# Performance work log

Hardware: AMD Instinct MI355X
Metric: run time of the kernel (lower is better)

Reference implementation:

```python
import jax, jax.numpy as jnp
import numpy as np

N = 100000   # nodes
E = 1000000  # edges
F = 128      # num_features
H = 64       # hidden_size
C = 1        # num_classes
G = 128      # num graphs in batch


def gcn_conv(x, W, b, src, dst, deg_inv_sqrt):
    # PyG GCNConv: add self-loops, symmetric normalization D^-1/2 (A+I) D^-1/2, then X W + b
    h = x @ W                                   # [N, H]
    norm = deg_inv_sqrt[src] * deg_inv_sqrt[dst]  # [E]
    msg = h[src] * norm[:, None]                # gather + scale, [E, H]
    out = jnp.zeros_like(h).at[dst].add(msg)    # scatter-add to targets
    out = out + h * (deg_inv_sqrt ** 2)[:, None]  # self-loop contribution
    return out + b


def setup_inputs() -> dict:
    key = jax.random.key(0)
    ks = jax.random.split(key, 12)
    x = jax.random.normal(ks[0], (N, F), dtype=jnp.float32)
    edge_index = jax.random.randint(ks[1], (2, E), 0, N, dtype=jnp.int32).astype(jnp.int64)
    batch = jnp.sort(jax.random.randint(ks[2], (N,), 0, G, dtype=jnp.int32)).astype(jnp.int64)
    def glorot(k, fan_in, fan_out):
        s = np.float32(np.sqrt(6.0 / (fan_in + fan_out)))
        return jax.random.uniform(k, (fan_in, fan_out), jnp.float32, -s, s)
    return {
        "x": x, "edge_index": edge_index, "batch": batch,
        "W1": glorot(ks[3], F, H), "b1": jnp.zeros((H,), jnp.float32),
        "W2": glorot(ks[4], H, H), "b2": jnp.zeros((H,), jnp.float32),
        "Wl1": glorot(ks[5], H, H), "bl1": jnp.zeros((H,), jnp.float32),
        "Wl2": glorot(ks[6], H, C), "bl2": jnp.zeros((C,), jnp.float32),
    }


def reference(x, edge_index, batch, W1, b1, W2, b2, Wl1, bl1, Wl2, bl2):
    src, dst = edge_index[0], edge_index[1]
    # degree with self-loops: 1 + in-degree(target)
    deg = jnp.ones((N,), x.dtype).at[dst].add(jnp.ones((E,), x.dtype))
    deg_inv_sqrt = jax.lax.rsqrt(deg)
    h = jax.nn.relu(gcn_conv(x, W1, b1, src, dst, deg_inv_sqrt))
    h = jax.nn.relu(gcn_conv(h, W2, b2, src, dst, deg_inv_sqrt))
    g = jax.ops.segment_sum(h, batch, num_segments=G)  # global_add_pool, [G, H]
    g = jax.nn.relu(g @ Wl1 + bl1)
    out = g @ Wl2 + bl2                                # [G, 1]
    return out.squeeze(axis=1)                         # [G]
```

## Files before the change

### kernel.cpp

```cpp
#include <hip/hip_runtime.h>

#define NN 100000
#define EE 1000000
#define FF 128
#define HH 64
#define GG 128
#define NB 391

__device__ inline unsigned short f2bf(float f) {
    unsigned u = __float_as_uint(f);
    u += 0x7fffu + ((u >> 16) & 1u);
    return (unsigned short)(u >> 16);
}
__device__ inline float bf2f(unsigned short h) {
    return __uint_as_float((unsigned)h << 16);
}

__global__ void k_hist(const int* __restrict__ ei, int* __restrict__ cnt) {
    int e = blockIdx.x * 256 + threadIdx.x;
    if (e < EE) atomicAdd(&cnt[ei[EE + e]], 1);
}

__global__ void k_scan1(const int* __restrict__ cnt, int* __restrict__ part) {
    int i = blockIdx.x * 256 + threadIdx.x;
    int v = (i < NN) ? cnt[i] : 0;
    for (int o = 1; o < 64; o <<= 1) v += __shfl_xor(v, o);
    __shared__ int ws[4];
    if ((threadIdx.x & 63) == 0) ws[threadIdx.x >> 6] = v;
    __syncthreads();
    if (threadIdx.x == 0) part[blockIdx.x] = ws[0] + ws[1] + ws[2] + ws[3];
}

__global__ void k_scan2(int* __restrict__ part) {
    __shared__ int buf[512];
    int t = threadIdx.x;
    int v = (t < NB) ? part[t] : 0;
    buf[t] = v; __syncthreads();
    for (int o = 1; o < 512; o <<= 1) {
        int u = (t >= o) ? buf[t - o] : 0;
        __syncthreads();
        buf[t] += u;
        __syncthreads();
    }
    if (t < NB) part[t] = buf[t] - v;
}

__global__ void k_scan3(const int* __restrict__ cnt, const int* __restrict__ part,
                        int* __restrict__ row_ptr, int* __restrict__ cursor,
                        float* __restrict__ dis) {
    int i = blockIdx.x * 256 + threadIdx.x;
    int v = (i < NN) ? cnt[i] : 0;
    int lane = threadIdx.x & 63, w = threadIdx.x >> 6;
    int incl = v;
    for (int o = 1; o < 64; o <<= 1) { int u = __shfl_up(incl, o); if (lane >= o) incl += u; }
    __shared__ int ws[4];
    if (lane == 63) ws[w] = incl;
    __syncthreads();
    int woff = 0;
    for (int k = 0; k < w; ++k) woff += ws[k];
    int excl = incl - v + woff + part[blockIdx.x];
    if (i < NN) {
        row_ptr[i] = excl;
        cursor[i]  = excl;
        dis[i] = rsqrtf((float)(v + 1));
    }
    if (i == 0) row_ptr[NN] = EE;
}

__global__ void k_place(const int* __restrict__ ei, int* __restrict__ cursor,
                        int* __restrict__ srcs) {
    int e = blockIdx.x * 256 + threadIdx.x;
    if (e < EE) {
        int d = ei[EE + e];
        int p = atomicAdd(&cursor[d], 1);
        srcs[p] = ei[e];
    }
}

template<int K>
__global__ __launch_bounds__(256) void
k_matmul_b(const float* __restrict__ X, const float* __restrict__ W,
           const float* __restrict__ dis, unsigned short* __restrict__ Y) {
    __shared__ float Wl[K * HH];
    for (int i = threadIdx.x; i < K * HH; i += 256) Wl[i] = W[i];
    __syncthreads();
    const int lane = threadIdx.x & 63;
    const int wv   = threadIdx.x >> 6;
    const int c4   = (lane & 15) * 4;
    const int rsg  = lane >> 4;
    const int r0   = blockIdx.x * 64 + wv * 16 + rsg * 4;

    const float* xr0; const float* xr1; const float* xr2; const float* xr3;
    {
        int a = r0,     b_ = r0 + 1, c = r0 + 2, d = r0 + 3;
        if (a > NN - 1) a = NN - 1;
        if (b_ > NN - 1) b_ = NN - 1;
        if (c > NN - 1) c = NN - 1;
        if (d > NN - 1) d = NN - 1;
        xr0 = X + (size_t)a * K; xr1 = X + (size_t)b_ * K;
        xr2 = X + (size_t)c * K; xr3 = X + (size_t)d * K;
    }
    float4 acc0 = {0,0,0,0}, acc1 = {0,0,0,0}, acc2 = {0,0,0,0}, acc3 = {0,0,0,0};

#pragma unroll 8
    for (int k4 = 0; k4 < K / 4; ++k4) {
        const float4 x0 = *(const float4*)(xr0 + k4 * 4);
        const float4 x1 = *(const float4*)(xr1 + k4 * 4);
        const float4 x2 = *(const float4*)(xr2 + k4 * 4);
        const float4 x3 = *(const float4*)(xr3 + k4 * 4);
        const float4 w0 = *(const float4*)&Wl[(k4 * 4 + 0) * HH + c4];
        const float4 w1 = *(const float4*)&Wl[(k4 * 4 + 1) * HH + c4];
        const float4 w2 = *(const float4*)&Wl[(k4 * 4 + 2) * HH + c4];
        const float4 w3 = *(const float4*)&Wl[(k4 * 4 + 3) * HH + c4];
#define FMA4(A, XS) \
        A.x = fmaf(XS.x, w0.x, A.x); A.y = fmaf(XS.x, w0.y, A.y); \
        A.z = fmaf(XS.x, w0.z, A.z); A.w = fmaf(XS.x, w0.w, A.w); \
        A.x = fmaf(XS.y, w1.x, A.x); A.y = fmaf(XS.y, w1.y, A.y); \
        A.z = fmaf(XS.y, w1.z, A.z); A.w = fmaf(XS.y, w1.w, A.w); \
        A.x = fmaf(XS.z, w2.x, A.x); A.y = fmaf(XS.z, w2.y, A.y); \
        A.z = fmaf(XS.z, w2.z, A.z); A.w = fmaf(XS.z, w2.w, A.w); \
        A.x = fmaf(XS.w, w3.x, A.x); A.y = fmaf(XS.w, w3.y, A.y); \
        A.z = fmaf(XS.w, w3.z, A.z); A.w = fmaf(XS.w, w3.w, A.w);
        FMA4(acc0, x0) FMA4(acc1, x1) FMA4(acc2, x2) FMA4(acc3, x3)
#undef FMA4
    }
#define STORE(I, A) { \
        const int r = r0 + I; \
        if (r < NN) { \
            const float d = dis[r]; \
            ushort4 o; \
            o.x = f2bf(A.x * d); o.y = f2bf(A.y * d); \
            o.z = f2bf(A.z * d); o.w = f2bf(A.w * d); \
            *(ushort4*)(Y + (size_t)r * HH + c4) = o; \
        } }
    STORE(0, acc0) STORE(1, acc1) STORE(2, acc2) STORE(3, acc3)
#undef STORE
}

template<bool POOL>
__global__ __launch_bounds__(256) void
k_gconv(const int* __restrict__ row_ptr, const int* __restrict__ srcs,
        const float* __restrict__ dis, const unsigned short* __restrict__ Hs,
        const float* __restrict__ b, float* __restrict__ Out,
        const int* __restrict__ batch, float* __restrict__ g) {
    const int node = blockIdx.x * 4 + (threadIdx.x >> 6);
    const int lane = threadIdx.x & 63;
    const int p1 = row_ptr[node + 1];
    int p = row_ptr[node];
    float a0 = 0.f, a1 = 0.f, a2 = 0.f, a3 = 0.f;
    int s0, s1, s2, s3;
    if (p + 4 <= p1) { s0 = srcs[p]; s1 = srcs[p+1]; s2 = srcs[p+2]; s3 = srcs[p+3]; }
    while (p + 4 <= p1) {
        const int q = p + 4;
        int t0, t1, t2, t3;
        if (q + 4 <= p1) { t0 = srcs[q]; t1 = srcs[q+1]; t2 = srcs[q+2]; t3 = srcs[q+3]; }
        a0 += bf2f(Hs[(size_t)s0 * HH + lane]);
        a1 += bf2f(Hs[(size_t)s1 * HH + lane]);
        a2 += bf2f(Hs[(size_t)s2 * HH + lane]);
        a3 += bf2f(Hs[(size_t)s3 * HH + lane]);
        s0 = t0; s1 = t1; s2 = t2; s3 = t3;
        p = q;
    }
    for (; p < p1; ++p) a0 += bf2f(Hs[(size_t)srcs[p] * HH + lane]);
    float acc = (a0 + a1) + (a2 + a3);
    const float dd = dis[node];
    float v = (acc + bf2f(Hs[(size_t)node * HH + lane])) * dd + b[lane];
    v = fmaxf(v, 0.0f);
    if (POOL) {
        unsafeAtomicAdd(&g[(size_t)batch[node] * HH + lane], v);
    } else {
        Out[(size_t)node * HH + lane] = v;
    }
}

__global__ void k_head1(const float* __restrict__ g, const float* __restrict__ W,
                        const float* __restrict__ b, float* __restrict__ g2) {
    const int idx = blockIdx.x * 256 + threadIdx.x;
    const int row = idx >> 6;
    const int col = idx & 63;
    const float* gr = g + (size_t)row * HH;
    float acc = b[col];
#pragma unroll
    for (int k = 0; k < HH; ++k) acc = fmaf(gr[k], W[k * HH + col], acc);
    g2[idx] = acc > 0.0f ? acc : 0.0f;
}

__global__ void k_head2(const float* __restrict__ g2, const float* __restrict__ W,
                        const float* __restrict__ b, float* __restrict__ out) {
    const int r = threadIdx.x;
    if (r >= GG) return;
    const float* gr = g2 + (size_t)r * HH;
    float acc = 0.0f;
#pragma unroll
    for (int k = 0; k < HH; ++k) acc = fmaf(gr[k], W[k], acc);
    out[r] = acc + b[0];
}

extern "C" void kernel_launch(void* const* d_in, const int* in_sizes, int n_in,
                              void* d_out, int out_size, void* d_ws, size_t ws_size,
                              hipStream_t stream) {
    const float* x   = (const float*)d_in[0];
    const int*   ei  = (const int*)d_in[1];
    const int*   bat = (const int*)d_in[2];
    const float* W1  = (const float*)d_in[3];
    const float* b1  = (const float*)d_in[4];
    const float* W2  = (const float*)d_in[5];
    const float* b2  = (const float*)d_in[6];
    const float* Wl1 = (const float*)d_in[7];
    const float* bl1 = (const float*)d_in[8];
    const float* Wl2 = (const float*)d_in[9];
    const float* bl2 = (const float*)d_in[10];
    float* out = (float*)d_out;

    char* w = (char*)d_ws;
    float* dis     = (float*)(w);
    int*   cnt     = (int*)  (w + 400128);
    int*   row_ptr = (int*)  (w + 800256);
    int*   cursor  = (int*)  (w + 1200640);
    int*   part    = (int*)  (w + 1600768);
    int*   srcs    = (int*)  (w + 1602816);
    unsigned short* B = (unsigned short*)(w + 5602816);
    float* A       = (float*)(w + 31202816);
    float* g       = (float*)(w + 56802816);
    float* g2      = g + GG * HH;

    hipMemsetAsync(cnt, 0, (size_t)NN * sizeof(int), stream);
    k_hist <<<(EE + 255) / 256, 256, 0, stream>>>(ei, cnt);
    k_scan1<<<NB, 256, 0, stream>>>(cnt, part);
    k_scan2<<<1, 512, 0, stream>>>(part);
    k_scan3<<<NB, 256, 0, stream>>>(cnt, part, row_ptr, cursor, dis);
    k_place<<<(EE + 255) / 256, 256, 0, stream>>>(ei, cursor, srcs);

    k_matmul_b<FF><<<(NN + 63) / 64, 256, 0, stream>>>(x, W1, dis, B);
    k_gconv<false><<<NN / 4, 256, 0, stream>>>(row_ptr, srcs, dis, B, b1, A, nullptr, nullptr);

    k_matmul_b<HH><<<(NN + 63) / 64, 256, 0, stream>>>(A, W2, dis, B);
    hipMemsetAsync(g, 0, (size_t)GG * HH * sizeof(float), stream);
    k_gconv<true><<<NN / 4, 256, 0, stream>>>(row_ptr, srcs, dis, B, b2, nullptr, bat, g);

    k_head1<<<(GG * HH) / 256, 256, 0, stream>>>(g, Wl1, bl1, g2);
    k_head2<<<1, 128, 0, stream>>>(g2, Wl2, bl2, out);
}
```

Before: 336.0 us.

## Gather neighbor rows with quarter-wave vector loads and software pipelining

Reorganizes the aggregation so each 16-lane quarter-wave loads a full bf16 row with 8-byte vector loads, processing 8 neighbor rows per batch with the self-loop folded in as an extra item. Index loads and row loads are pipelined one batch ahead, then partial sums are combined with cross-lane shuffles. This aims to raise memory-level parallelism and load width for the random-gather-bound aggregation, at the cost of shuffle reduction overhead and masked wasted loads for low-degree nodes.

```diff
diff --git a/kernel.cpp b/kernel.cpp
--- a/kernel.cpp
+++ b/kernel.cpp
@@ -145,26 +145,66 @@
         const int* __restrict__ batch, float* __restrict__ g) {
     const int node = blockIdx.x * 4 + (threadIdx.x >> 6);
     const int lane = threadIdx.x & 63;
-    const int p1 = row_ptr[node + 1];
-    int p = row_ptr[node];
-    float a0 = 0.f, a1 = 0.f, a2 = 0.f, a3 = 0.f;
-    int s0, s1, s2, s3;
-    if (p + 4 <= p1) { s0 = srcs[p]; s1 = srcs[p+1]; s2 = srcs[p+2]; s3 = srcs[p+3]; }
-    while (p + 4 <= p1) {
-        const int q = p + 4;
-        int t0, t1, t2, t3;
-        if (q + 4 <= p1) { t0 = srcs[q]; t1 = srcs[q+1]; t2 = srcs[q+2]; t3 = srcs[q+3]; }
-        a0 += bf2f(Hs[(size_t)s0 * HH + lane]);
-        a1 += bf2f(Hs[(size_t)s1 * HH + lane]);
-        a2 += bf2f(Hs[(size_t)s2 * HH + lane]);
-        a3 += bf2f(Hs[(size_t)s3 * HH + lane]);
-        s0 = t0; s1 = t1; s2 = t2; s3 = t3;
-        p = q;
-    }
-    for (; p < p1; ++p) a0 += bf2f(Hs[(size_t)srcs[p] * HH + lane]);
-    float acc = (a0 + a1) + (a2 + a3);
+    const int li   = lane & 15;
+    const int qr   = lane >> 4;
+    const int p0   = row_ptr[node];
+    const int deg  = row_ptr[node + 1] - p0;
+    const int items  = deg + 1;
+    const int nbatch = (items + 7) >> 3;
+
+    float ac0 = 0.f, ac1 = 0.f, ac2 = 0.f, ac3 = 0.f;
+
+#define IDX(bi, dA, dB) { \
+        const int iA = 8 * (bi) + qr, iB = iA + 4; \
+        dA = srcs[p0 + (iA < deg ? iA : 0)]; \
+        dB = srcs[p0 + (iB < deg ? iB : 0)]; }
+#define VAL(bi, sA, sB, vA, vB) { \
+        const int iA = 8 * (bi) + qr, iB = iA + 4; \
+        const int rA = (iA < deg) ? sA : node; \
+        const int rB = (iB < deg) ? sB : node; \
+        vA = *(const uint2*)(Hs + (size_t)rA * HH + li * 4); \
+        vB = *(const uint2*)(Hs + (size_t)rB * HH + li * 4); }
+#define CONSUME(bi, vA, vB) { \
+        const int iA = 8 * (bi) + qr, iB = iA + 4; \
+        const unsigned m0 = (iA <= deg) ? vA.x : 0u; \
+        const unsigned m1 = (iA <= deg) ? vA.y : 0u; \
+        const unsigned m2 = (iB <= deg) ? vB.x : 0u; \
+        const unsigned m3 = (iB <= deg) ? vB.y : 0u; \
+        ac0 += bf2f((unsigned short)m0);  ac1 += bf2f((unsigned short)(m0 >> 16)); \
+        ac2 += bf2f((unsigned short)m1);  ac3 += bf2f((unsigned short)(m1 >> 16)); \
+        ac0 += bf2f((unsigned short)m2);  ac1 += bf2f((unsigned short)(m2 >> 16)); \
+        ac2 += bf2f((unsigned short)m3);  ac3 += bf2f((unsigned short)(m3 >> 16)); }
+
+    int sA0, sA1, sB0, sB1;
+    uint2 vA0, vA1;
+    IDX(0, sA0, sA1);
+    VAL(0, sA0, sA1, vA0, vA1);
+    IDX(1, sB0, sB1);
+    for (int bi = 1; bi < nbatch; ++bi) {
+        uint2 vB0, vB1;
+        VAL(bi, sB0, sB1, vB0, vB1);
+        IDX(bi + 1, sB0, sB1);
+        CONSUME(bi - 1, vA0, vA1);
+        vA0 = vB0; vA1 = vB1;
+    }
+    CONSUME(nbatch - 1, vA0, vA1);
+#undef IDX
+#undef VAL
+#undef CONSUME
+
+    ac0 += __shfl_xor(ac0, 16); ac0 += __shfl_xor(ac0, 32);
+    ac1 += __shfl_xor(ac1, 16); ac1 += __shfl_xor(ac1, 32);
+    ac2 += __shfl_xor(ac2, 16); ac2 += __shfl_xor(ac2, 32);
+    ac3 += __shfl_xor(ac3, 16); ac3 += __shfl_xor(ac3, 32);
+    const float c0 = __shfl(ac0, lane >> 2);
+    const float c1 = __shfl(ac1, lane >> 2);
+    const float c2 = __shfl(ac2, lane >> 2);
+    const float c3 = __shfl(ac3, lane >> 2);
+    const int m = lane & 3;
+    float acc = (m == 0) ? c0 : (m == 1) ? c1 : (m == 2) ? c2 : c3;
+
     const float dd = dis[node];
-    float v = (acc + bf2f(Hs[(size_t)node * HH + lane])) * dd + b[lane];
+    float v = acc * dd + b[lane];
     v = fmaxf(v, 0.0f);
     if (POOL) {
         unsafeAtomicAdd(&g[(size_t)batch[node] * HH + lane], v);
```

Result: faster. 319.6 us (-4.9%).

## Pad CSR rows to multiples of four and gather bf16 rows 16 lanes per node

Applied to the files above, without the earlier changes.

The CSR rows are padded to a multiple of four slots. Each row gets the node itself as the self-loop entry, and the rest is filled with a zero dummy row at index NN. The aggregation kernel now handles 16 nodes per block with 16 lanes per node, each lane loading 4 bf16 values (uint2). It stages up to 32 source indices in shared memory and issues up to 32 independent gathers before consuming any, so there are more loads in flight and no tail loop. The costs are extra padded slots, a larger unrolled register footprint, and pooling that now uses four atomics per lane.

```diff
diff --git a/kernel.cpp b/kernel.cpp
--- a/kernel.cpp
+++ b/kernel.cpp
@@ -12,18 +12,17 @@
     u += 0x7fffu + ((u >> 16) & 1u);
     return (unsigned short)(u >> 16);
 }
-__device__ inline float bf2f(unsigned short h) {
-    return __uint_as_float((unsigned)h << 16);
-}
 
 __global__ void k_hist(const int* __restrict__ ei, int* __restrict__ cnt) {
     int e = blockIdx.x * 256 + threadIdx.x;
     if (e < EE) atomicAdd(&cnt[ei[EE + e]], 1);
 }
 
-__global__ void k_scan1(const int* __restrict__ cnt, int* __restrict__ part) {
+__global__ void k_scan1(const int* __restrict__ cnt, int* __restrict__ part,
+                        unsigned short* __restrict__ B) {
+    if (blockIdx.x == 0 && threadIdx.x < HH) B[(size_t)NN * HH + threadIdx.x] = 0;
     int i = blockIdx.x * 256 + threadIdx.x;
-    int v = (i < NN) ? cnt[i] : 0;
+    int v = (i < NN) ? ((cnt[i] + 4) & ~3) : 0;
     for (int o = 1; o < 64; o <<= 1) v += __shfl_xor(v, o);
     __shared__ int ws[4];
     if ((threadIdx.x & 63) == 0) ws[threadIdx.x >> 6] = v;
@@ -47,9 +46,11 @@
 
 __global__ void k_scan3(const int* __restrict__ cnt, const int* __restrict__ part,
                         int* __restrict__ row_ptr, int* __restrict__ cursor,
-                        float* __restrict__ dis) {
+                        int* __restrict__ srcs, float* __restrict__ dis) {
     int i = blockIdx.x * 256 + threadIdx.x;
-    int v = (i < NN) ? cnt[i] : 0;
+    int c = (i < NN) ? cnt[i] : 0;
+    int slots = (c + 4) & ~3;
+    int v = (i < NN) ? slots : 0;
     int lane = threadIdx.x & 63, w = threadIdx.x >> 6;
     int incl = v;
     for (int o = 1; o < 64; o <<= 1) { int u = __shfl_up(incl, o); if (lane >= o) incl += u; }
@@ -61,10 +62,12 @@
     int excl = incl - v + woff + part[blockIdx.x];
     if (i < NN) {
         row_ptr[i] = excl;
-        cursor[i]  = excl;
-        dis[i] = rsqrtf((float)(v + 1));
-    }
-    if (i == 0) row_ptr[NN] = EE;
+        cursor[i]  = excl + 1;
+        srcs[excl] = i;
+        for (int t = c + 1; t < slots; ++t) srcs[excl + t] = NN;
+        dis[i] = rsqrtf((float)(c + 1));
+        if (i == NN - 1) row_ptr[NN] = excl + slots;
+    }
 }
 
 __global__ void k_place(const int* __restrict__ ei, int* __restrict__ cursor,
@@ -137,39 +140,69 @@
 #undef STORE
 }
 
+#define AW(w) __uint_as_float((w) << 16)
+#define AH(w) __uint_as_float((w) & 0xffff0000u)
 template<bool POOL>
 __global__ __launch_bounds__(256) void
 k_gconv(const int* __restrict__ row_ptr, const int* __restrict__ srcs,
         const float* __restrict__ dis, const unsigned short* __restrict__ Hs,
         const float* __restrict__ b, float* __restrict__ Out,
         const int* __restrict__ batch, float* __restrict__ g) {
-    const int node = blockIdx.x * 4 + (threadIdx.x >> 6);
-    const int lane = threadIdx.x & 63;
-    const int p1 = row_ptr[node + 1];
-    int p = row_ptr[node];
-    float a0 = 0.f, a1 = 0.f, a2 = 0.f, a3 = 0.f;
-    int s0, s1, s2, s3;
-    if (p + 4 <= p1) { s0 = srcs[p]; s1 = srcs[p+1]; s2 = srcs[p+2]; s3 = srcs[p+3]; }
-    while (p + 4 <= p1) {
-        const int q = p + 4;
-        int t0, t1, t2, t3;
-        if (q + 4 <= p1) { t0 = srcs[q]; t1 = srcs[q+1]; t2 = srcs[q+2]; t3 = srcs[q+3]; }
-        a0 += bf2f(Hs[(size_t)s0 * HH + lane]);
-        a1 += bf2f(Hs[(size_t)s1 * HH + lane]);
-        a2 += bf2f(Hs[(size_t)s2 * HH + lane]);
-        a3 += bf2f(Hs[(size_t)s3 * HH + lane]);
-        s0 = t0; s1 = t1; s2 = t2; s3 = t3;
-        p = q;
-    }
-    for (; p < p1; ++p) a0 += bf2f(Hs[(size_t)srcs[p] * HH + lane]);
-    float acc = (a0 + a1) + (a2 + a3);
+    __shared__ int L[16 * 32];
+    const int grp  = threadIdx.x >> 4;
+    const int li   = threadIdx.x & 15;
+    const int node = blockIdx.x * 16 + grp;
+    const int p0   = row_ptr[node];
+    const int pend = row_ptr[node + 1];
+    const int slots = pend - p0;
+    const int nbc  = (slots >> 2) < 8 ? (slots >> 2) : 8;
+    int* Lg = L + grp * 32;
+    for (int q = li; q < 32; q += 16)
+        if (q < slots) Lg[q] = srcs[p0 + q];
+    __syncthreads();
+
+    float4 acc = {0.f, 0.f, 0.f, 0.f};
+    uint2 r00,r01,r02,r03,r10,r11,r12,r13,r20,r21,r22,r23,r30,r31,r32,r33,
+          r40,r41,r42,r43,r50,r51,r52,r53,r60,r61,r62,r63,r70,r71,r72,r73;
+#define ISSUE(K,R0,R1,R2,R3) if (K < nbc) { \
+    const size_t i0=Lg[4*K+0], i1=Lg[4*K+1], i2=Lg[4*K+2], i3=Lg[4*K+3]; \
+    R0 = *(const uint2*)(Hs + i0*HH + li*4); \
+    R1 = *(const uint2*)(Hs + i1*HH + li*4); \
+    R2 = *(const uint2*)(Hs + i2*HH + li*4); \
+    R3 = *(const uint2*)(Hs + i3*HH + li*4); }
+    ISSUE(0,r00,r01,r02,r03) ISSUE(1,r10,r11,r12,r13)
+    ISSUE(2,r20,r21,r22,r23) ISSUE(3,r30,r31,r32,r33)
+    ISSUE(4,r40,r41,r42,r43) ISSUE(5,r50,r51,r52,r53)
+    ISSUE(6,r60,r61,r62,r63) ISSUE(7,r70,r71,r72,r73)
+#undef ISSUE
+#define CONS(K,R0,R1,R2,R3) if (K < nbc) { \
+    acc.x += AW(R0.x) + AW(R1.x) + AW(R2.x) + AW(R3.x); \
+    acc.y += AH(R0.x) + AH(R1.x) + AH(R2.x) + AH(R3.x); \
+    acc.z += AW(R0.y) + AW(R1.y) + AW(R2.y) + AW(R3.y); \
+    acc.w += AH(R0.y) + AH(R1.y) + AH(R2.y) + AH(R3.y); }
+    CONS(0,r00,r01,r02,r03) CONS(1,r10,r11,r12,r13)
+    CONS(2,r20,r21,r22,r23) CONS(3,r30,r31,r32,r33)
+    CONS(4,r40,r41,r42,r43) CONS(5,r50,r51,r52,r53)
+    CONS(6,r60,r61,r62,r63) CONS(7,r70,r71,r72,r73)
+#undef CONS
+    for (int q = p0 + 32; q < pend; ++q) {
+        const size_t s = srcs[q];
+        uint2 v = *(const uint2*)(Hs + s * HH + li * 4);
+        acc.x += AW(v.x); acc.y += AH(v.x); acc.z += AW(v.y); acc.w += AH(v.y);
+    }
     const float dd = dis[node];
-    float v = (acc + bf2f(Hs[(size_t)node * HH + lane])) * dd + b[lane];
-    v = fmaxf(v, 0.0f);
+    const float4 bv = *(const float4*)(b + li * 4);
+    float4 v;
+    v.x = fmaxf(fmaf(acc.x, dd, bv.x), 0.f);
+    v.y = fmaxf(fmaf(acc.y, dd, bv.y), 0.f);
+    v.z = fmaxf(fmaf(acc.z, dd, bv.z), 0.f);
+    v.w = fmaxf(fmaf(acc.w, dd, bv.w), 0.f);
     if (POOL) {
-        unsafeAtomicAdd(&g[(size_t)batch[node] * HH + lane], v);
+        float* gp = g + (size_t)batch[node] * HH + li * 4;
+        unsafeAtomicAdd(gp + 0, v.x); unsafeAtomicAdd(gp + 1, v.y);
+        unsafeAtomicAdd(gp + 2, v.z); unsafeAtomicAdd(gp + 3, v.w);
     } else {
-        Out[(size_t)node * HH + lane] = v;
+        *(float4*)(Out + (size_t)node * HH + li * 4) = v;
     }
 }
 
@@ -219,24 +252,24 @@
     int*   cursor  = (int*)  (w + 1200640);
     int*   part    = (int*)  (w + 1600768);
     int*   srcs    = (int*)  (w + 1602816);
-    unsigned short* B = (unsigned short*)(w + 5602816);
-    float* A       = (float*)(w + 31202816);
-    float* g       = (float*)(w + 56802816);
+    unsigned short* B = (unsigned short*)(w + 7602816);
+    float* A       = (float*)(w + 20403200);
+    float* g       = (float*)(w + 46003200);
     float* g2      = g + GG * HH;
 
     hipMemsetAsync(cnt, 0, (size_t)NN * sizeof(int), stream);
     k_hist <<<(EE + 255) / 256, 256, 0, stream>>>(ei, cnt);
-    k_scan1<<<NB, 256, 0, stream>>>(cnt, part);
+    k_scan1<<<NB, 256, 0, stream>>>(cnt, part, B);
     k_scan2<<<1, 512, 0, stream>>>(part);
-    k_scan3<<<NB, 256, 0, stream>>>(cnt, part, row_ptr, cursor, dis);
+    k_scan3<<<NB, 256, 0, stream>>>(cnt, part, row_ptr, cursor, srcs, dis);
     k_place<<<(EE + 255) / 256, 256, 0, stream>>>(ei, cursor, srcs);
 
     k_matmul_b<FF><<<(NN + 63) / 64, 256, 0, stream>>>(x, W1, dis, B);
-    k_gconv<false><<<NN / 4, 256, 0, stream>>>(row_ptr, srcs, dis, B, b1, A, nullptr, nullptr);
+    k_gconv<false><<<NN / 16, 256, 0, stream>>>(row_ptr, srcs, dis, B, b1, A, nullptr, nullptr);
 
     k_matmul_b<HH><<<(NN + 63) / 64, 256, 0, stream>>>(A, W2, dis, B);
     hipMemsetAsync(g, 0, (size_t)GG * HH * sizeof(float), stream);
-    k_gconv<true><<<NN / 4, 256, 0, stream>>>(row_ptr, srcs, dis, B, b2, nullptr, bat, g);
+    k_gconv<true><<<NN / 16, 256, 0, stream>>>(row_ptr, srcs, dis, B, b2, nullptr, bat, g);
 
     k_head1<<<(GG * HH) / 256, 256, 0, stream>>>(g, Wl1, bl1, g2);
     k_head2<<<1, 128, 0, stream>>>(g2, Wl2, bl2, out);
```

Result: slower. 496.5 us (+47.8%).
